# Kernel tuning notes

Measured on AMD Instinct MI355X. Metric: run time of the kernel, lower is better.

## Reference

```python
import jax, jax.numpy as jnp
import numpy as np

PAD_VALUE = 0.0


def setup_inputs() -> dict:
    key = jax.random.key(0)
    k1, k2 = jax.random.split(key)
    B, DIM, T = 16, 384, 512
    x = jax.random.normal(k1, (B, DIM, T), dtype=jnp.float32)
    duration = jax.random.randint(k2, (B, T), 0, 8, dtype=jnp.int32)
    return {"x": x, "duration": duration, "d_max": T * 8}


def reference(x, duration, d_max):
    """Length regulator (FastSpeech-style).

    x:        (B, dim, T) float32
    duration: (B, T) int32, frames per input timestep
    d_max:    static int, padded output frame length (>= max total duration)

    Returns:
      out:     (B, dim, d_max) expanded/padded tensor
      mel_len: (B,) int32 true output lengths
    """
    B, dim, T = x.shape
    # Guard against all-zero duration rows (original fills them with 1s).
    row_sum = duration.sum(axis=1)  # (B,)
    duration = jnp.where((row_sum == 0)[:, None], jnp.ones_like(duration), duration)

    cum = jnp.cumsum(duration, axis=1)  # (B, T) exclusive-end offsets
    mel_len = cum[:, -1]  # (B,)

    frames = jnp.arange(d_max, dtype=jnp.int32)  # (d_max,)
    # Source index for each output frame: first t with cum[t] > frame.
    idx = jax.vmap(lambda c: jnp.searchsorted(c, frames, side="right"))(cum)  # (B, d_max)
    idx = jnp.clip(idx, 0, T - 1)

    out = jnp.take_along_axis(x, idx[:, None, :], axis=2)  # (B, dim, d_max)
    valid = frames[None, :] < mel_len[:, None]  # (B, d_max)
    out = jnp.where(valid[:, None, :], out, jnp.asarray(PAD_VALUE, x.dtype))
    return out, mel_len
```

## Files before the change

### kernel.cpp

```cpp
#include <hip/hip_runtime.h>

#define B_SZ   16
#define DIM_SZ 384
#define T_SZ   512
#define DMAX   4096
#define DC     8
#define FC     2048

__global__ __launch_bounds__(64) void lr_scan_kernel(const int* __restrict__ duration,
                                                     unsigned short* __restrict__ ws_idx,
                                                     int* __restrict__ ws_mel,
                                                     float* __restrict__ mel_out) {
    const int b = blockIdx.x;
    const int l = threadIdx.x;
    const int4* __restrict__ src = (const int4*)(duration + b * T_SZ);
    const int4 a = src[l * 2];
    const int4 c = src[l * 2 + 1];
    int p[8];
    p[0] = a.x;        p[1] = p[0] + a.y; p[2] = p[1] + a.z; p[3] = p[2] + a.w;
    p[4] = p[3] + c.x; p[5] = p[4] + c.y; p[6] = p[5] + c.z; p[7] = p[6] + c.w;
    int s = p[7];
#pragma unroll
    for (int off = 1; off < 64; off <<= 1) {
        const int v = __shfl_up(s, off);
        if (l >= off) s += v;
    }
    const int excl   = s - p[7];
    const int rowsum = __shfl(s, 63);
    unsigned short* __restrict__ idxb = ws_idx + b * DMAX;
    if (rowsum == 0) {
        const int t0 = l * 8;
        ushort4* dst = (ushort4*)(idxb + t0);
        dst[0] = make_ushort4((unsigned short)(t0 + 0), (unsigned short)(t0 + 1),
                              (unsigned short)(t0 + 2), (unsigned short)(t0 + 3));
        dst[1] = make_ushort4((unsigned short)(t0 + 4), (unsigned short)(t0 + 5),
                              (unsigned short)(t0 + 6), (unsigned short)(t0 + 7));
        if (l == 63) { ws_mel[b] = T_SZ; mel_out[b] = (float)T_SZ; }
    } else {
        int start = excl;
#pragma unroll
        for (int k = 0; k < 8; ++k) {
            const unsigned short t = (unsigned short)(l * 8 + k);
            const int e = excl + p[k];
            for (int f = start; f < e; ++f) idxb[f] = t;
            start = e;
        }
        if (l == 63) { ws_mel[b] = rowsum; mel_out[b] = (float)rowsum; }
    }
}

__global__ __launch_bounds__(256) void lr_gather_kernel(const float* __restrict__ x,
                                                        const unsigned short* __restrict__ ws_idx,
                                                        const int* __restrict__ ws_mel,
                                                        float* __restrict__ out) {
    __shared__ float s_x[DC * T_SZ];
    const int tid = threadIdx.x;
    const int b   = blockIdx.y;
    const int d0  = blockIdx.z * DC;
    const int f0  = blockIdx.x * FC;
    const int mel = ws_mel[b];
    float4* __restrict__ outp = (float4*)(out + (size_t)b * DIM_SZ * DMAX);

    if (f0 >= mel) {
        const float4 z = make_float4(0.f, 0.f, 0.f, 0.f);
#pragma unroll
        for (int g = 0; g < FC / 1024; ++g) {
            const int f4 = ((f0 + g * 1024) >> 2) + tid;
#pragma unroll
            for (int dd = 0; dd < DC; ++dd)
                outp[(size_t)(d0 + dd) * (DMAX / 4) + f4] = z;
        }
        return;
    }

    const float4* __restrict__ xsrc = (const float4*)(x + ((size_t)b * DIM_SZ + d0) * T_SZ);
    float4* s_x4 = (float4*)s_x;
#pragma unroll
    for (int i = 0; i < (DC * T_SZ / 4) / 256; ++i)
        s_x4[i * 256 + tid] = xsrc[i * 256 + tid];
    __syncthreads();

    const ushort4* __restrict__ idxp = (const ushort4*)(ws_idx + (size_t)b * DMAX);

#pragma unroll
    for (int g = 0; g < FC / 1024; ++g) {
        const int f  = f0 + g * 1024 + tid * 4;
        const int f4 = f >> 2;
        if (f >= mel) {
            const float4 z = make_float4(0.f, 0.f, 0.f, 0.f);
#pragma unroll
            for (int dd = 0; dd < DC; ++dd)
                outp[(size_t)(d0 + dd) * (DMAX / 4) + f4] = z;
        } else {
            const ushort4 i4 = idxp[f4];
            int idx[4] = { i4.x & (T_SZ - 1), i4.y & (T_SZ - 1),
                           i4.z & (T_SZ - 1), i4.w & (T_SZ - 1) };
            bool valid[4];
#pragma unroll
            for (int j = 0; j < 4; ++j) valid[j] = (f + j < mel);
#pragma unroll
            for (int dd = 0; dd < DC; ++dd) {
                const float* __restrict__ xr = s_x + dd * T_SZ;
                float4 v;
                v.x = valid[0] ? xr[idx[0]] : 0.0f;
                v.y = valid[1] ? xr[idx[1]] : 0.0f;
                v.z = valid[2] ? xr[idx[2]] : 0.0f;
                v.w = valid[3] ? xr[idx[3]] : 0.0f;
                outp[(size_t)(d0 + dd) * (DMAX / 4) + f4] = v;
            }
        }
    }
}

extern "C" void kernel_launch(void* const* d_in, const int* in_sizes, int n_in,
                              void* d_out, int out_size, void* d_ws, size_t ws_size,
                              hipStream_t stream) {
    const float* x        = (const float*)d_in[0];
    const int*   duration = (const int*)d_in[1];

    float* out     = (float*)d_out;
    float* mel_out = out + (size_t)B_SZ * DIM_SZ * DMAX;

    unsigned short* ws_idx = (unsigned short*)d_ws;
    int* ws_mel = (int*)((char*)d_ws + (size_t)B_SZ * DMAX * sizeof(unsigned short));

    lr_scan_kernel<<<B_SZ, 64, 0, stream>>>(duration, ws_idx, ws_mel, mel_out);

    dim3 grid(DMAX / FC, B_SZ, DIM_SZ / DC);
    lr_gather_kernel<<<grid, 256, 0, stream>>>(x, ws_idx, ws_mel, out);
}
```

Before: 118.1 us.

## Fuse duration scan into gather kernel with per-block shared-memory index table

Removes the separate scan kernel and its global workspace. Each gather block recomputes the prefix sum of its batch row and fills a shared-memory index table covering only its own frame window. Blocks with f0==0 start loading x into shared memory before the scan so the two overlap. The cost is that the scan is repeated in every block, and the scatter into shared memory is serialized per lane.

```diff
diff --git a/kernel.cpp b/kernel.cpp
--- a/kernel.cpp
+++ b/kernel.cpp
@@ -7,58 +7,76 @@
 #define DC     8
 #define FC     2048
 
-__global__ __launch_bounds__(64) void lr_scan_kernel(const int* __restrict__ duration,
-                                                     unsigned short* __restrict__ ws_idx,
-                                                     int* __restrict__ ws_mel,
-                                                     float* __restrict__ mel_out) {
-    const int b = blockIdx.x;
-    const int l = threadIdx.x;
-    const int4* __restrict__ src = (const int4*)(duration + b * T_SZ);
-    const int4 a = src[l * 2];
-    const int4 c = src[l * 2 + 1];
-    int p[8];
-    p[0] = a.x;        p[1] = p[0] + a.y; p[2] = p[1] + a.z; p[3] = p[2] + a.w;
-    p[4] = p[3] + c.x; p[5] = p[4] + c.y; p[6] = p[5] + c.z; p[7] = p[6] + c.w;
-    int s = p[7];
-#pragma unroll
-    for (int off = 1; off < 64; off <<= 1) {
-        const int v = __shfl_up(s, off);
-        if (l >= off) s += v;
-    }
-    const int excl   = s - p[7];
-    const int rowsum = __shfl(s, 63);
-    unsigned short* __restrict__ idxb = ws_idx + b * DMAX;
-    if (rowsum == 0) {
-        const int t0 = l * 8;
-        ushort4* dst = (ushort4*)(idxb + t0);
-        dst[0] = make_ushort4((unsigned short)(t0 + 0), (unsigned short)(t0 + 1),
-                              (unsigned short)(t0 + 2), (unsigned short)(t0 + 3));
-        dst[1] = make_ushort4((unsigned short)(t0 + 4), (unsigned short)(t0 + 5),
-                              (unsigned short)(t0 + 6), (unsigned short)(t0 + 7));
-        if (l == 63) { ws_mel[b] = T_SZ; mel_out[b] = (float)T_SZ; }
-    } else {
-        int start = excl;
-#pragma unroll
-        for (int k = 0; k < 8; ++k) {
-            const unsigned short t = (unsigned short)(l * 8 + k);
-            const int e = excl + p[k];
-            for (int f = start; f < e; ++f) idxb[f] = t;
-            start = e;
-        }
-        if (l == 63) { ws_mel[b] = rowsum; mel_out[b] = (float)rowsum; }
-    }
-}
-
-__global__ __launch_bounds__(256) void lr_gather_kernel(const float* __restrict__ x,
-                                                        const unsigned short* __restrict__ ws_idx,
-                                                        const int* __restrict__ ws_mel,
-                                                        float* __restrict__ out) {
+__global__ __launch_bounds__(256) void lr_fused_kernel(const float* __restrict__ x,
+                                                       const int* __restrict__ duration,
+                                                       float* __restrict__ out,
+                                                       float* __restrict__ mel_out) {
     __shared__ float s_x[DC * T_SZ];
+    __shared__ unsigned short s_idx[FC];
+    __shared__ int s_mel;
     const int tid = threadIdx.x;
     const int b   = blockIdx.y;
     const int d0  = blockIdx.z * DC;
     const int f0  = blockIdx.x * FC;
-    const int mel = ws_mel[b];
+
+    const float4* __restrict__ xsrc = (const float4*)(x + ((size_t)b * DIM_SZ + d0) * T_SZ);
+    float4* s_x4 = (float4*)s_x;
+    const bool eager = (f0 == 0);
+    if (eager) {
+#pragma unroll
+        for (int i = 0; i < (DC * T_SZ / 4) / 256; ++i)
+            s_x4[i * 256 + tid] = xsrc[i * 256 + tid];
+    }
+
+    if (tid < 64) {
+        const int l = tid;
+        const int4* __restrict__ src = (const int4*)(duration + b * T_SZ);
+        const int4 a = src[l * 2];
+        const int4 c = src[l * 2 + 1];
+        int p[8];
+        p[0] = a.x;        p[1] = p[0] + a.y; p[2] = p[1] + a.z; p[3] = p[2] + a.w;
+        p[4] = p[3] + c.x; p[5] = p[4] + c.y; p[6] = p[5] + c.z; p[7] = p[6] + c.w;
+        int s = p[7];
+#pragma unroll
+        for (int off = 1; off < 64; off <<= 1) {
+            const int v = __shfl_up(s, off);
+            if (l >= off) s += v;
+        }
+        const int excl   = s - p[7];
+        const int rowsum = __shfl(s, 63);
+        if (rowsum == 0) {
+            if (f0 == 0) {
+                const int t0 = l * 8;
+                ushort4* dst = (ushort4*)(s_idx + t0);
+                dst[0] = make_ushort4((unsigned short)(t0 + 0), (unsigned short)(t0 + 1),
+                                      (unsigned short)(t0 + 2), (unsigned short)(t0 + 3));
+                dst[1] = make_ushort4((unsigned short)(t0 + 4), (unsigned short)(t0 + 5),
+                                      (unsigned short)(t0 + 6), (unsigned short)(t0 + 7));
+            }
+            if (l == 63) {
+                s_mel = T_SZ;
+                if (blockIdx.x == 0 && blockIdx.z == 0) mel_out[b] = (float)T_SZ;
+            }
+        } else {
+            int start = excl;
+#pragma unroll
+            for (int k = 0; k < 8; ++k) {
+                const unsigned short t = (unsigned short)(l * 8 + k);
+                const int e  = excl + p[k];
+                const int lo = start < f0 ? f0 : start;
+                const int hi = e > f0 + FC ? f0 + FC : e;
+                for (int f = lo; f < hi; ++f) s_idx[f - f0] = t;
+                start = e;
+            }
+            if (l == 63) {
+                s_mel = rowsum;
+                if (blockIdx.x == 0 && blockIdx.z == 0) mel_out[b] = (float)rowsum;
+            }
+        }
+    }
+    __syncthreads();
+
+    const int mel = s_mel;
     float4* __restrict__ outp = (float4*)(out + (size_t)b * DIM_SZ * DMAX);
 
     if (f0 >= mel) {
@@ -72,15 +90,12 @@
         }
         return;
     }
-
-    const float4* __restrict__ xsrc = (const float4*)(x + ((size_t)b * DIM_SZ + d0) * T_SZ);
-    float4* s_x4 = (float4*)s_x;
+    if (!eager) {
 #pragma unroll
-    for (int i = 0; i < (DC * T_SZ / 4) / 256; ++i)
-        s_x4[i * 256 + tid] = xsrc[i * 256 + tid];
-    __syncthreads();
-
-    const ushort4* __restrict__ idxp = (const ushort4*)(ws_idx + (size_t)b * DMAX);
+        for (int i = 0; i < (DC * T_SZ / 4) / 256; ++i)
+            s_x4[i * 256 + tid] = xsrc[i * 256 + tid];
+        __syncthreads();
+    }
 
 #pragma unroll
     for (int g = 0; g < FC / 1024; ++g) {
@@ -92,7 +107,7 @@
             for (int dd = 0; dd < DC; ++dd)
                 outp[(size_t)(d0 + dd) * (DMAX / 4) + f4] = z;
         } else {
-            const ushort4 i4 = idxp[f4];
+            const ushort4 i4 = ((const ushort4*)s_idx)[g * 256 + tid];
             int idx[4] = { i4.x & (T_SZ - 1), i4.y & (T_SZ - 1),
                            i4.z & (T_SZ - 1), i4.w & (T_SZ - 1) };
             bool valid[4];
@@ -120,12 +135,8 @@
 
     float* out     = (float*)d_out;
     float* mel_out = out + (size_t)B_SZ * DIM_SZ * DMAX;
-
-    unsigned short* ws_idx = (unsigned short*)d_ws;
-    int* ws_mel = (int*)((char*)d_ws + (size_t)B_SZ * DMAX * sizeof(unsigned short));
-
-    lr_scan_kernel<<<B_SZ, 64, 0, stream>>>(duration, ws_idx, ws_mel, mel_out);
+    (void)d_ws; (void)ws_size;
 
     dim3 grid(DMAX / FC, B_SZ, DIM_SZ / DC);
-    lr_gather_kernel<<<grid, 256, 0, stream>>>(x, ws_idx, ws_mel, out);
+    lr_fused_kernel<<<grid, 256, 0, stream>>>(x, duration, out, mel_out);
 }
```

Result: faster. 115.2 us (median of 2 runs) (-2.5%).
